# Performance work log

Measured on AMD Instinct MI355X. Metric: run time of the kernel, lower is better.

## Reference

```python
import jax, jax.numpy as jnp
import numpy as np

N = 100_000      # nodes
E = 1_600_000    # edges (avg degree 16)
H = 4            # heads
C = 32           # per-head channels
HID = 128        # hidden = H*C
L = 4            # layers
IN, ED, OUT = 8, 6, 256
NEG_SLOPE = 0.2  # LeakyReLU default in GATv2Conv


def setup_inputs() -> dict:
    key = jax.random.key(0)
    ks = jax.random.split(key, 16)
    s = 0.1
    return {
        "x": jax.random.normal(ks[0], (N, IN), dtype=jnp.float32),
        "edge_index": jax.random.randint(ks[1], (2, E), 0, N, dtype=jnp.int32),
        "edge_attr": jax.random.normal(ks[2], (E, ED), dtype=jnp.float32),
        "W_in": jax.random.normal(ks[3], (IN, HID), dtype=jnp.float32) * s,
        "b_in": jnp.zeros((HID,), jnp.float32),
        "W_l": jax.random.normal(ks[4], (L, HID, HID), dtype=jnp.float32) * s,
        "b_l": jnp.zeros((L, HID), jnp.float32),
        "W_r": jax.random.normal(ks[5], (L, HID, HID), dtype=jnp.float32) * s,
        "b_r": jnp.zeros((L, HID), jnp.float32),
        "W_e": jax.random.normal(ks[6], (L, ED, HID), dtype=jnp.float32) * s,
        "att": jax.random.normal(ks[7], (L, H, C), dtype=jnp.float32) * s,
        "bias": jnp.zeros((L, HID), jnp.float32),
        "ln_w": jnp.ones((L, HID), jnp.float32),
        "ln_b": jnp.zeros((L, HID), jnp.float32),
        "W_out": jax.random.normal(ks[8], (HID, OUT), dtype=jnp.float32) * s,
        "b_out": jnp.zeros((OUT,), jnp.float32),
    }


def _elu(x):
    return jnp.where(x > 0, x, jnp.expm1(x))


def _leaky(x):
    return jnp.where(x > 0, x, NEG_SLOPE * x)


def _layernorm(x, w, b):
    mu = jnp.mean(x, axis=-1, keepdims=True)
    var = jnp.var(x, axis=-1, keepdims=True)
    return (x - mu) * jax.lax.rsqrt(var + 1e-5) * w + b


def _forward(x, edge_index, edge_attr, W_in, b_in, W_l, b_l, W_r, b_r,
             W_e, att, bias, ln_w, ln_b, W_out, b_out):
    src, dst = edge_index[0], edge_index[1]
    # add_self_loops with fill_value='mean': self-loop edge_attr = mean of incoming edge_attr
    deg = jax.ops.segment_sum(jnp.ones((E,), x.dtype), dst, num_segments=N)
    loop_attr = jax.ops.segment_sum(edge_attr, dst, num_segments=N) / jnp.maximum(deg, 1.0)[:, None]
    loops = jnp.arange(N, dtype=src.dtype)
    src_a = jnp.concatenate([src, loops])          # [E+N]
    dst_a = jnp.concatenate([dst, loops])          # [E+N]
    eattr_a = jnp.concatenate([edge_attr, loop_attr], axis=0)  # [E+N, ED]

    h = _elu(x @ W_in + b_in)  # [N, HID]
    for i in range(L):
        res = h
        xl = (h @ W_l[i] + b_l[i]).reshape(N, H, C)   # source transform
        xr = (h @ W_r[i] + b_r[i]).reshape(N, H, C)   # target transform
        ea = (eattr_a @ W_e[i]).reshape(-1, H, C)     # edge transform
        m = _leaky(xl[src_a] + xr[dst_a] + ea)        # [E+N, H, C]
        score = jnp.einsum('ehc,hc->eh', m, att[i])   # [E+N, H]
        # segment softmax over incoming edges per target node
        smax = jax.ops.segment_max(score, dst_a, num_segments=N)[dst_a]
        ex = jnp.exp(score - smax)
        denom = jax.ops.segment_sum(ex, dst_a, num_segments=N)[dst_a]
        alpha = ex / denom                             # [E+N, H]
        out = jax.ops.segment_sum(alpha[:, :, None] * xl[src_a], dst_a,
                                  num_segments=N).reshape(N, HID) + bias[i]
        h = _elu(_layernorm(out + res, ln_w[i], ln_b[i]))
        # dropout: identity (eval mode)
    return h @ W_out + b_out  # [N, OUT]


def reference(x, edge_index, edge_attr, W_in, b_in, W_l, b_l, W_r, b_r,
              W_e, att, bias, ln_w, ln_b, W_out, b_out):
    return _forward(x, edge_index, edge_attr, W_in, b_in, W_l, b_l, W_r, b_r,
                    W_e, att, bias, ln_w, ln_b, W_out, b_out)
```

## Files before the change

kernel.cpp:

```cpp
#include <hip/hip_runtime.h>
#include <hip/hip_bf16.h>
#include <hip/hip_fp16.h>

#define N_NODES 100000
#define N_EDGES 1600000
#define HEADS 4
#define CHN 32
#define HID 128
#define LAYERS 4
#define IN_F 8
#define ED_F 6
#define OUT_F 256
#define NEG_SLOPE 0.2f

#define NT_GEMM ((N_NODES + 63) / 64)
#define GRID_GEMM 512

typedef _Float16 f16x8 __attribute__((ext_vector_type(8)));
typedef _Float16 f16x4 __attribute__((ext_vector_type(4)));
typedef _Float16 h2 __attribute__((ext_vector_type(2)));
typedef float f32x4 __attribute__((ext_vector_type(4)));

#if defined(__has_builtin)
#if __has_builtin(__builtin_amdgcn_fdot2)
#define HAVE_FDOT2 1
#endif
#endif

__device__ __forceinline__ float elu_f(float x) {
    return x > 0.f ? x : expm1f(x);
}

__device__ __forceinline__ h2 bith2(float f) {
    union { float f; h2 h; } u; u.f = f; return u.h;
}

__device__ __forceinline__ float dot6(h2 e01, h2 e23, h2 e45, const h2* w) {
#ifdef HAVE_FDOT2
    return __builtin_amdgcn_fdot2(e45, w[2],
           __builtin_amdgcn_fdot2(e23, w[1],
           __builtin_amdgcn_fdot2(e01, w[0], 0.f, false), false), false);
#else
    float s = (float)e01[0] * (float)w[0][0];
    s = fmaf((float)e01[1], (float)w[0][1], s);
    s = fmaf((float)e23[0], (float)w[1][0], s);
    s = fmaf((float)e23[1], (float)w[1][1], s);
    s = fmaf((float)e45[0], (float)w[2][0], s);
    s = fmaf((float)e45[1], (float)w[2][1], s);
    return s;
#endif
}


__global__ void hist_kernel(const int* __restrict__ dst, int* __restrict__ fill) {
    int e = blockIdx.x * blockDim.x + threadIdx.x;
    if (e < N_EDGES) atomicAdd(&fill[dst[e]], 1);
}

__global__ void scan1_kernel(const int* __restrict__ cnt, int* __restrict__ bsum) {
    __shared__ int sd[256];
    int t = threadIdx.x;
    int base = blockIdx.x * 1024 + t * 4;
    int s = 0;
#pragma unroll
    for (int j = 0; j < 4; ++j) {
        int i = base + j;
        if (i < N_NODES) s += cnt[i];
    }
    sd[t] = s;
    for (int off = 128; off > 0; off >>= 1) {
        __syncthreads();
        if (t < off) sd[t] += sd[t + off];
    }
    if (t == 0) bsum[blockIdx.x] = sd[0];
}

__global__ void scan2_kernel(int* __restrict__ bsum, int* __restrict__ rowptr, int nb) {
    __shared__ int sd[256];
    int t = threadIdx.x;
    int v = (t < nb) ? bsum[t] : 0;
    sd[t] = v;
    __syncthreads();
    for (int off = 1; off < 256; off <<= 1) {
        int x = (t >= off) ? sd[t - off] : 0;
        __syncthreads();
        sd[t] += x;
        __syncthreads();
    }
    if (t < nb) bsum[t] = sd[t] - v;
    if (t == 0) rowptr[N_NODES] = sd[255];
}

__global__ void scan3_kernel(const int* __restrict__ cnt, const int* __restrict__ bsum,
                             int* __restrict__ rowptr) {
    __shared__ int sd[256];
    int t = threadIdx.x;
    int base = blockIdx.x * 1024 + t * 4;
    int v[4];
#pragma unroll
    for (int j = 0; j < 4; ++j) {
        int i = base + j;
        v[j] = (i < N_NODES) ? cnt[i] : 0;
    }
    int s = v[0] + v[1] + v[2] + v[3];
    sd[t] = s;
    __syncthreads();
    for (int off = 1; off < 256; off <<= 1) {
        int xv = (t >= off) ? sd[t - off] : 0;
        __syncthreads();
        sd[t] += xv;
        __syncthreads();
    }
    int excl = sd[t] - s + bsum[blockIdx.x];
    int pre = 0;
#pragma unroll
    for (int j = 0; j < 4; ++j) {
        int i = base + j;
        if (i < N_NODES) rowptr[i] = excl + pre;
        pre += v[j];
    }
}

__global__ void fill_kernel(const int* __restrict__ src, const int* __restrict__ dst,
                            const int* __restrict__ rowptr, int* __restrict__ fill,
                            int2* __restrict__ csr) {
    int e = blockIdx.x * blockDim.x + threadIdx.x;
    if (e >= N_EDGES) return;
    int d = dst[e];
    int p = rowptr[d] + atomicAdd(&fill[d], 1);
    csr[p] = make_int2(src[e] * 512, e * 16);
}

__global__ void ecvt_kernel(const float* __restrict__ eattr, __half* __restrict__ ea16) {
    int gid = blockIdx.x * blockDim.x + threadIdx.x;
    if (gid >= N_EDGES * 8) return;
    int e = gid >> 3, d = gid & 7;
    float v = (d < ED_F) ? eattr[e * ED_F + d] : 0.f;
    ea16[gid] = __float2half_rn(v);
}

__global__ void lattr_kernel(const int* __restrict__ rowptr, const int2* __restrict__ csr,
                             const __half* __restrict__ ea16, __half* __restrict__ lat16) {
    int gid = blockIdx.x * blockDim.x + threadIdx.x;
    if (gid >= N_NODES * 8) return;
    int n = gid >> 3;
    int d = gid & 7;
    float s = 0.f;
    if (d < ED_F) {
        int rp0 = rowptr[n], rp1 = rowptr[n + 1];
        for (int p = rp0; p < rp1; ++p) {
            int eid = csr[p].y >> 4;
            s += (float)ea16[(size_t)eid * 8 + d];
        }
        int deg = rp1 - rp0;
        s /= (float)(deg > 0 ? deg : 1);
    }
    lat16[gid] = __float2half_rn(s);
}


__global__ void convw_kernel(const float* __restrict__ W_l, const float* __restrict__ W_r,
                             const float* __restrict__ W_out, __half* __restrict__ wbt) {
    int gid = blockIdx.x * blockDim.x + threadIdx.x;
    if (gid >= 5 * 256 * 128) return;
    int b = gid >> 15;
    int idx = gid & 32767;
    int n = idx >> 7, k = idx & 127;
    float val;
    if (b < 4)
        val = (n < HID) ? W_l[b * HID * HID + k * HID + n]
                        : W_r[b * HID * HID + k * HID + (n - HID)];
    else
        val = W_out[k * OUT_F + n];
    int boff = n * 256 + ((k * 2) ^ ((n & 7) << 4));
    *(__half*)((char*)wbt + (size_t)b * 65536 + boff) = __float2half_rn(val);
}


__global__ void in_kernel(const float* __restrict__ x, const float* __restrict__ Wi,
                          const float* __restrict__ bi, __half* __restrict__ h16) {
    int gid = blockIdx.x * blockDim.x + threadIdx.x;
    if (gid >= N_NODES * HID) return;
    int n = gid >> 7, j = gid & 127;
    float acc = bi[j];
#pragma unroll
    for (int k = 0; k < IN_F; ++k) acc = fmaf(x[n * IN_F + k], Wi[k * HID + j], acc);
    h16[gid] = __float2half_rn(elu_f(acc));
}


#define LDS_B_OFF 16384

template <int MODE>
__global__ __launch_bounds__(256, 2) void gemm_kernel(
    const __half* __restrict__ A16, const __half* __restrict__ Bt,
    const float* __restrict__ bias0, const float* __restrict__ bias1,
    __half* __restrict__ xlr16, float* __restrict__ outp) {
    __shared__ __align__(16) unsigned char smem[81920];
    int t = threadIdx.x;

#pragma unroll
    for (int it = 0; it < 16; ++it) {
        int off = (it * 256 + t) * 16;
        *(float4*)(smem + LDS_B_OFF + off) = *(const float4*)((const char*)Bt + off);
    }

    int wave = t >> 6;
    int lane = t & 63;
    int lc = lane & 15, lr = lane >> 4;
    int cbase = wave * 64;

    for (int tile = blockIdx.x; tile < NT_GEMM; tile += GRID_GEMM) {
        int row0 = tile * 64;
#pragma unroll
        for (int it = 0; it < 4; ++it) {
            int idx = it * 256 + t;
            int r = idx >> 4;
            int kb = (idx & 15) * 16;
            f16x8 p = *(const f16x8*)((const char*)A16 + (size_t)(row0 + r) * 256 + kb);
            *(f16x8*)(smem + r * 256 + (kb ^ ((r & 7) << 4))) = p;
        }
        __syncthreads();

        f32x4 acc[4][4];
#pragma unroll
        for (int i = 0; i < 4; ++i)
#pragma unroll
            for (int j = 0; j < 4; ++j) acc[i][j] = (f32x4){0.f, 0.f, 0.f, 0.f};

#pragma unroll
        for (int kk = 0; kk < 4; ++kk) {
            int kb = kk * 64 + lr * 16;
            f16x8 av[4], bv[4];
#pragma unroll
            for (int rt = 0; rt < 4; ++rt) {
                int r = rt * 16 + lc;
                av[rt] = *(const f16x8*)(smem + r * 256 + (kb ^ ((r & 7) << 4)));
            }
#pragma unroll
            for (int ct = 0; ct < 4; ++ct) {
                int c = cbase + ct * 16 + lc;
                bv[ct] = *(const f16x8*)(smem + LDS_B_OFF + c * 256 + (kb ^ ((c & 7) << 4)));
            }
#pragma unroll
            for (int rt = 0; rt < 4; ++rt)
#pragma unroll
                for (int ct = 0; ct < 4; ++ct)
                    acc[rt][ct] = __builtin_amdgcn_mfma_f32_16x16x32_f16(av[rt], bv[ct],
                                                                         acc[rt][ct], 0, 0, 0);
        }
        __syncthreads();

#pragma unroll
        for (int ct = 0; ct < 4; ++ct) {
            int col = cbase + ct * 16 + lc;
            float bv;
            if (MODE == 0) bv = (col < HID) ? bias0[col] : bias1[col - HID];
            else bv = bias0[col];
#pragma unroll
            for (int rt = 0; rt < 4; ++rt) {
#pragma unroll
                for (int q = 0; q < 4; ++q) {
                    int node = row0 + rt * 16 + lr * 4 + q;
                    if (node < N_NODES) {
                        float val = acc[rt][ct][q] + bv;
                        if (MODE == 0)
                            xlr16[(size_t)node * 256 + col] = __float2half_rn(val);
                        else
                            outp[(size_t)node * OUT_F + col] = val;
                    }
                }
            }
        }
    }
}


struct Slot {
    float4 er;
    float2 xv;
};

__device__ __forceinline__ void slot_issue(Slot& s, int i, int total, int rp0,
                                           const int2* __restrict__ csr,
                                           const char* eab, const char* lat16v,
                                           const char* xlb, int vbytes) {
    i = min(i, total - 1);
    const char* eb;
    const char* xb;
    if (i == 0) {
        eb = lat16v;
        xb = xlb + (size_t)vbytes;
    } else {
        int2 se = csr[rp0 + i - 1];
        eb = eab + (size_t)se.y;
        xb = xlb + (size_t)se.x;
    }
    s.er = *(const float4*)eb;
    s.xv = *(const float2*)xb;
}

__device__ __forceinline__ void slot_consume(const Slot& sl, int i, int total,
                                             const h2 we_h2[4][3], const float* attv,
                                             const float* xrv,
                                             float& denom, float* acc) {
    h2 e01 = bith2(sl.er.x), e23 = bith2(sl.er.y), e45 = bith2(sl.er.z);
    h2 x01 = bith2(sl.xv.x), x23 = bith2(sl.xv.y);
    float xf[4];
    xf[0] = (float)x01[0]; xf[1] = (float)x01[1];
    xf[2] = (float)x23[0]; xf[3] = (float)x23[1];
    float t = 0.f;
#pragma unroll
    for (int c = 0; c < 4; ++c) {
        float ea = dot6(e01, e23, e45, we_h2[c]);
        float m = xf[c] + xrv[c] + ea;
        m = m > 0.f ? m : NEG_SLOPE * m;
        t = fmaf(m, attv[c], t);
    }
    t += __shfl_xor(t, 1);
    t += __shfl_xor(t, 2);
    t += __shfl_xor(t, 4);
    float ex = __expf(t);
    ex = (i < total) ? ex : 0.f;
    denom += ex;
#pragma unroll
    for (int c = 0; c < 4; ++c) acc[c] = fmaf(ex, xf[c], acc[c]);
}

__global__ __launch_bounds__(64, 8) void edge_kernel(
    const __half* __restrict__ xlr16,
    __half* __restrict__ h16,
    const int* __restrict__ rowptr, const int2* __restrict__ csr,
    const __half* __restrict__ ea16, const __half* __restrict__ lat16,
    const float* __restrict__ We, const float* __restrict__ att,
    const float* __restrict__ bias_l, const float* __restrict__ lnw,
    const float* __restrict__ lnb) {
    int v = blockIdx.x;
    int lane = threadIdx.x;
    int half = lane >> 5;
    int hl = lane & 31;
    int c0 = hl * 4;

    h2 we_h2[4][3];
#pragma unroll
    for (int c = 0; c < 4; ++c)
#pragma unroll
        for (int d = 0; d < 3; ++d) {
            h2 w;
            w[0] = (_Float16)We[(2 * d) * HID + c0 + c];
            w[1] = (_Float16)We[(2 * d + 1) * HID + c0 + c];
            we_h2[c][d] = w;
        }
    float4 at4 = *(const float4*)(att + c0);
    float attv[4] = {at4.x, at4.y, at4.z, at4.w};
    float xrv[4];
    {
        float2 xraw = *(const float2*)(xlr16 + (size_t)v * 256 + 128 + c0);
        h2 xr01 = bith2(xraw.x), xr23 = bith2(xraw.y);
        xrv[0] = (float)xr01[0]; xrv[1] = (float)xr01[1];
        xrv[2] = (float)xr23[0]; xrv[3] = (float)xr23[1];
    }

    int rp0 = rowptr[v], rp1 = rowptr[v + 1];
    int total = (rp1 - rp0) + 1;
    int R = (total + 1) >> 1;

    const char* xlb = (const char*)xlr16 + (size_t)c0 * 2;
    const char* eab = (const char*)ea16;
    const char* lat16v = (const char*)lat16 + (size_t)v * 16;
    int vbytes = v * 512;

    float denom = 0.f;
    float acc[4] = {0.f, 0.f, 0.f, 0.f};

    Slot sA, sB;
    slot_issue(sA, half, total, rp0, csr, eab, lat16v, xlb, vbytes);
    if (R > 1) slot_issue(sB, 2 + half, total, rp0, csr, eab, lat16v, xlb, vbytes);
    int r = 0;
    for (; r + 2 <= R; r += 2) {
        slot_consume(sA, 2 * r + half, total, we_h2, attv, xrv, denom, acc);
        if (r + 2 < R) slot_issue(sA, 2 * (r + 2) + half, total, rp0, csr, eab, lat16v, xlb, vbytes);
        slot_consume(sB, 2 * (r + 1) + half, total, we_h2, attv, xrv, denom, acc);
        if (r + 3 < R) slot_issue(sB, 2 * (r + 3) + half, total, rp0, csr, eab, lat16v, xlb, vbytes);
    }
    if (r < R) slot_consume(sA, 2 * r + half, total, we_h2, attv, xrv, denom, acc);

    denom += __shfl_xor(denom, 32);
#pragma unroll
    for (int c = 0; c < 4; ++c) acc[c] += __shfl_xor(acc[c], 32);

    float rd = 1.f / denom;

    float2 rb = *(const float2*)(h16 + (size_t)v * HID + c0);
    h2 r01 = bith2(rb.x), r23 = bith2(rb.y);
    float4 bv4 = *(const float4*)(bias_l + c0);
    float y[4];
    y[0] = acc[0] * rd + bv4.x + (float)r01[0];
    y[1] = acc[1] * rd + bv4.y + (float)r01[1];
    y[2] = acc[2] * rd + bv4.z + (float)r23[0];
    y[3] = acc[3] * rd + bv4.w + (float)r23[1];
    float s = y[0] + y[1] + y[2] + y[3];
    float sq = fmaf(y[0], y[0], fmaf(y[1], y[1], fmaf(y[2], y[2], y[3] * y[3])));
#pragma unroll
    for (int off = 1; off < 32; off <<= 1) {
        s += __shfl_xor(s, off);
        sq += __shfl_xor(sq, off);
    }
    float mu = s * (1.f / HID);
    float var = sq * (1.f / HID) - mu * mu;
    float rstd = rsqrtf(var + 1e-5f);
    float4 wv4 = *(const float4*)(lnw + c0);
    float4 lb4 = *(const float4*)(lnb + c0);
    if (half == 0) {
        f16x4 o;
        o[0] = (_Float16)elu_f((y[0] - mu) * rstd * wv4.x + lb4.x);
        o[1] = (_Float16)elu_f((y[1] - mu) * rstd * wv4.y + lb4.y);
        o[2] = (_Float16)elu_f((y[2] - mu) * rstd * wv4.z + lb4.z);
        o[3] = (_Float16)elu_f((y[3] - mu) * rstd * wv4.w + lb4.w);
        *(f16x4*)(h16 + (size_t)v * HID + c0) = o;
    }
}


extern "C" void kernel_launch(void* const* d_in, const int* in_sizes, int n_in,
                              void* d_out, int out_size, void* d_ws, size_t ws_size,
                              hipStream_t stream) {
    const float* x     = (const float*)d_in[0];
    const int*   ei    = (const int*)d_in[1];
    const float* eattr = (const float*)d_in[2];
    const float* W_in  = (const float*)d_in[3];
    const float* b_in  = (const float*)d_in[4];
    const float* W_l   = (const float*)d_in[5];
    const float* b_l   = (const float*)d_in[6];
    const float* W_r   = (const float*)d_in[7];
    const float* b_r   = (const float*)d_in[8];
    const float* W_e   = (const float*)d_in[9];
    const float* att   = (const float*)d_in[10];
    const float* bias  = (const float*)d_in[11];
    const float* lnw   = (const float*)d_in[12];
    const float* lnb   = (const float*)d_in[13];
    const float* W_out = (const float*)d_in[14];
    const float* b_out = (const float*)d_in[15];
    float* out = (float*)d_out;

    __half* h16   = (__half*)d_ws;
    __half* lat16 = h16 + (size_t)N_NODES * HID;
    int* rowptr   = (int*)(lat16 + (size_t)N_NODES * 8);
    int* fill     = rowptr + (N_NODES + 4);
    int2* csr     = (int2*)(fill + N_NODES);
    int* bsum     = (int*)(csr + N_EDGES);
    __half* wbt   = (__half*)(bsum + 256);

    __half* xlr16 = (__half*)out;
    __half* ea16  = xlr16 + (size_t)N_NODES * 256;

    const int* srcv = ei;
    const int* dstv = ei + N_EDGES;

    hipMemsetAsync(fill, 0, N_NODES * sizeof(int), stream);
    hist_kernel<<<(N_EDGES + 255) / 256, 256, 0, stream>>>(dstv, fill);
    int nb = (N_NODES + 1023) / 1024;
    scan1_kernel<<<nb, 256, 0, stream>>>(fill, bsum);
    scan2_kernel<<<1, 256, 0, stream>>>(bsum, rowptr, nb);
    scan3_kernel<<<nb, 256, 0, stream>>>(fill, bsum, rowptr);
    hipMemsetAsync(fill, 0, N_NODES * sizeof(int), stream);
    fill_kernel<<<(N_EDGES + 255) / 256, 256, 0, stream>>>(srcv, dstv, rowptr, fill, csr);
    ecvt_kernel<<<(N_EDGES * 8 + 255) / 256, 256, 0, stream>>>(eattr, ea16);
    lattr_kernel<<<(N_NODES * 8 + 255) / 256, 256, 0, stream>>>(rowptr, csr, ea16, lat16);

    convw_kernel<<<(5 * 256 * 128 + 255) / 256, 256, 0, stream>>>(W_l, W_r, W_out, wbt);
    in_kernel<<<(N_NODES * HID) / 256, 256, 0, stream>>>(x, W_in, b_in, h16);

    for (int l = 0; l < LAYERS; ++l) {
        gemm_kernel<0><<<GRID_GEMM, 256, 0, stream>>>(
            h16, wbt + (size_t)l * 32768, b_l + (size_t)l * HID, b_r + (size_t)l * HID,
            xlr16, nullptr);
        edge_kernel<<<N_NODES, 64, 0, stream>>>(
            xlr16, h16, rowptr, csr, ea16, lat16,
            W_e + (size_t)l * ED_F * HID, att + (size_t)l * HEADS * CHN,
            bias + (size_t)l * HID, lnw + (size_t)l * HID, lnb + (size_t)l * HID);
    }

    gemm_kernel<1><<<GRID_GEMM, 256, 0, stream>>>(
        h16, wbt + (size_t)4 * 32768, b_out, nullptr, nullptr, out);
}
```

Measured before the change: 925.4 us.

## Compute GATv2 edge message math in packed fp16 with duplicated edge attributes

Edge attributes are now stored with each feature value duplicated as a half2 pair (32 bytes per edge), so the edge kernel can form the message with packed fp16 multiply-adds over channel pairs. The older form did one fdot2 per channel. LeakyReLU becomes a packed max, the attention dot uses fdot2, and the softmax uses exp2 with log2(e) folded into the attention weights. This cuts per-edge ALU work in the edge kernel. In exchange, the edge-attribute buffer doubles in size and each edge costs extra gather bandwidth, and the pre-activation sum is accumulated in fp16, which loses precision.

```diff
diff --git a/kernel.cpp b/kernel.cpp
--- a/kernel.cpp
+++ b/kernel.cpp
@@ -35,19 +35,11 @@
     union { float f; h2 h; } u; u.f = f; return u.h;
 }
 
-__device__ __forceinline__ float dot6(h2 e01, h2 e23, h2 e45, const h2* w) {
+__device__ __forceinline__ float fdot2f(h2 a, h2 b, float c) {
 #ifdef HAVE_FDOT2
-    return __builtin_amdgcn_fdot2(e45, w[2],
-           __builtin_amdgcn_fdot2(e23, w[1],
-           __builtin_amdgcn_fdot2(e01, w[0], 0.f, false), false), false);
+    return __builtin_amdgcn_fdot2(a, b, c, false);
 #else
-    float s = (float)e01[0] * (float)w[0][0];
-    s = fmaf((float)e01[1], (float)w[0][1], s);
-    s = fmaf((float)e23[0], (float)w[1][0], s);
-    s = fmaf((float)e23[1], (float)w[1][1], s);
-    s = fmaf((float)e45[0], (float)w[2][0], s);
-    s = fmaf((float)e45[1], (float)w[2][1], s);
-    return s;
+    return fmaf((float)a[1], (float)b[1], fmaf((float)a[0], (float)b[0], c));
 #endif
 }
 
@@ -128,13 +120,13 @@
     if (e >= N_EDGES) return;
     int d = dst[e];
     int p = rowptr[d] + atomicAdd(&fill[d], 1);
-    csr[p] = make_int2(src[e] * 512, e * 16);
+    csr[p] = make_int2(src[e] * 512, e * 32);
 }
 
 __global__ void ecvt_kernel(const float* __restrict__ eattr, __half* __restrict__ ea16) {
     int gid = blockIdx.x * blockDim.x + threadIdx.x;
-    if (gid >= N_EDGES * 8) return;
-    int e = gid >> 3, d = gid & 7;
+    if (gid >= N_EDGES * 16) return;
+    int e = gid >> 4, d = (gid & 15) >> 1;
     float v = (d < ED_F) ? eattr[e * ED_F + d] : 0.f;
     ea16[gid] = __float2half_rn(v);
 }
@@ -142,15 +134,16 @@
 __global__ void lattr_kernel(const int* __restrict__ rowptr, const int2* __restrict__ csr,
                              const __half* __restrict__ ea16, __half* __restrict__ lat16) {
     int gid = blockIdx.x * blockDim.x + threadIdx.x;
-    if (gid >= N_NODES * 8) return;
-    int n = gid >> 3;
-    int d = gid & 7;
+    if (gid >= N_NODES * 16) return;
+    int n = gid >> 4;
+    int j = gid & 15;
+    int d = j >> 1;
     float s = 0.f;
     if (d < ED_F) {
         int rp0 = rowptr[n], rp1 = rowptr[n + 1];
         for (int p = rp0; p < rp1; ++p) {
-            int eid = csr[p].y >> 4;
-            s += (float)ea16[(size_t)eid * 8 + d];
+            int eid = csr[p].y >> 5;
+            s += (float)ea16[(size_t)eid * 16 + 2 * d];
         }
         int deg = rp1 - rp0;
         s /= (float)(deg > 0 ? deg : 1);
@@ -277,7 +270,8 @@
 
 
 struct Slot {
-    float4 er;
+    float4 er0;
+    float2 er1;
     float2 xv;
 };
 
@@ -296,35 +290,38 @@
         eb = eab + (size_t)se.y;
         xb = xlb + (size_t)se.x;
     }
-    s.er = *(const float4*)eb;
+    s.er0 = *(const float4*)eb;
+    s.er1 = *(const float2*)(eb + 16);
     s.xv = *(const float2*)xb;
 }
 
 __device__ __forceinline__ void slot_consume(const Slot& sl, int i, int total,
-                                             const h2 we_h2[4][3], const float* attv,
-                                             const float* xrv,
-                                             float& denom, float* acc) {
-    h2 e01 = bith2(sl.er.x), e23 = bith2(sl.er.y), e45 = bith2(sl.er.z);
-    h2 x01 = bith2(sl.xv.x), x23 = bith2(sl.xv.y);
-    float xf[4];
-    xf[0] = (float)x01[0]; xf[1] = (float)x01[1];
-    xf[2] = (float)x23[0]; xf[3] = (float)x23[1];
-    float t = 0.f;
-#pragma unroll
-    for (int c = 0; c < 4; ++c) {
-        float ea = dot6(e01, e23, e45, we_h2[c]);
-        float m = xf[c] + xrv[c] + ea;
-        m = m > 0.f ? m : NEG_SLOPE * m;
-        t = fmaf(m, attv[c], t);
-    }
+                                             const h2 w2[6][2], const h2* att2,
+                                             const h2* xr2, float& denom, float* acc) {
+    h2 xl0 = bith2(sl.xv.x), xl1 = bith2(sl.xv.y);
+    h2 sp0 = xl0 + xr2[0];
+    h2 sp1 = xl1 + xr2[1];
+    h2 es;
+    es = bith2(sl.er0.x); sp0 += es * w2[0][0]; sp1 += es * w2[0][1];
+    es = bith2(sl.er0.y); sp0 += es * w2[1][0]; sp1 += es * w2[1][1];
+    es = bith2(sl.er0.z); sp0 += es * w2[2][0]; sp1 += es * w2[2][1];
+    es = bith2(sl.er0.w); sp0 += es * w2[3][0]; sp1 += es * w2[3][1];
+    es = bith2(sl.er1.x); sp0 += es * w2[4][0]; sp1 += es * w2[4][1];
+    es = bith2(sl.er1.y); sp0 += es * w2[5][0]; sp1 += es * w2[5][1];
+    const h2 kns = {(_Float16)NEG_SLOPE, (_Float16)NEG_SLOPE};
+    h2 l0 = __builtin_elementwise_max(sp0, sp0 * kns);
+    h2 l1 = __builtin_elementwise_max(sp1, sp1 * kns);
+    float t = fdot2f(l1, att2[1], fdot2f(l0, att2[0], 0.f));
     t += __shfl_xor(t, 1);
     t += __shfl_xor(t, 2);
     t += __shfl_xor(t, 4);
-    float ex = __expf(t);
+    float ex = exp2f(t);
     ex = (i < total) ? ex : 0.f;
     denom += ex;
-#pragma unroll
-    for (int c = 0; c < 4; ++c) acc[c] = fmaf(ex, xf[c], acc[c]);
+    acc[0] = fmaf((float)xl0[0], ex, acc[0]);
+    acc[1] = fmaf((float)xl0[1], ex, acc[1]);
+    acc[2] = fmaf((float)xl1[0], ex, acc[2]);
+    acc[3] = fmaf((float)xl1[1], ex, acc[3]);
 }
 
 __global__ __launch_bounds__(64, 8) void edge_kernel(
@@ -341,24 +338,29 @@
     int hl = lane & 31;
     int c0 = hl * 4;
 
-    h2 we_h2[4][3];
-#pragma unroll
-    for (int c = 0; c < 4; ++c)
-#pragma unroll
-        for (int d = 0; d < 3; ++d) {
+    h2 w2[6][2];
+#pragma unroll
+    for (int d = 0; d < 6; ++d)
+#pragma unroll
+        for (int p = 0; p < 2; ++p) {
             h2 w;
-            w[0] = (_Float16)We[(2 * d) * HID + c0 + c];
-            w[1] = (_Float16)We[(2 * d + 1) * HID + c0 + c];
-            we_h2[c][d] = w;
+            w[0] = (_Float16)We[d * HID + c0 + 2 * p];
+            w[1] = (_Float16)We[d * HID + c0 + 2 * p + 1];
+            w2[d][p] = w;
         }
-    float4 at4 = *(const float4*)(att + c0);
-    float attv[4] = {at4.x, at4.y, at4.z, at4.w};
-    float xrv[4];
+    const float L2E = 1.44269504f;
+    h2 att2[2];
+    {
+        float4 a = *(const float4*)(att + c0);
+        h2 t0, t1;
+        t0[0] = (_Float16)(a.x * L2E); t0[1] = (_Float16)(a.y * L2E);
+        t1[0] = (_Float16)(a.z * L2E); t1[1] = (_Float16)(a.w * L2E);
+        att2[0] = t0; att2[1] = t1;
+    }
+    h2 xr2[2];
     {
         float2 xraw = *(const float2*)(xlr16 + (size_t)v * 256 + 128 + c0);
-        h2 xr01 = bith2(xraw.x), xr23 = bith2(xraw.y);
-        xrv[0] = (float)xr01[0]; xrv[1] = (float)xr01[1];
-        xrv[2] = (float)xr23[0]; xrv[3] = (float)xr23[1];
+        xr2[0] = bith2(xraw.x); xr2[1] = bith2(xraw.y);
     }
 
     int rp0 = rowptr[v], rp1 = rowptr[v + 1];
@@ -367,7 +369,7 @@
 
     const char* xlb = (const char*)xlr16 + (size_t)c0 * 2;
     const char* eab = (const char*)ea16;
-    const char* lat16v = (const char*)lat16 + (size_t)v * 16;
+    const char* lat16v = (const char*)lat16 + (size_t)v * 32;
     int vbytes = v * 512;
 
     float denom = 0.f;
@@ -378,12 +380,12 @@
     if (R > 1) slot_issue(sB, 2 + half, total, rp0, csr, eab, lat16v, xlb, vbytes);
     int r = 0;
     for (; r + 2 <= R; r += 2) {
-        slot_consume(sA, 2 * r + half, total, we_h2, attv, xrv, denom, acc);
+        slot_consume(sA, 2 * r + half, total, w2, att2, xr2, denom, acc);
         if (r + 2 < R) slot_issue(sA, 2 * (r + 2) + half, total, rp0, csr, eab, lat16v, xlb, vbytes);
-        slot_consume(sB, 2 * (r + 1) + half, total, we_h2, attv, xrv, denom, acc);
+        slot_consume(sB, 2 * (r + 1) + half, total, w2, att2, xr2, denom, acc);
         if (r + 3 < R) slot_issue(sB, 2 * (r + 3) + half, total, rp0, csr, eab, lat16v, xlb, vbytes);
     }
-    if (r < R) slot_consume(sA, 2 * r + half, total, we_h2, attv, xrv, denom, acc);
+    if (r < R) slot_consume(sA, 2 * r + half, total, w2, att2, xr2, denom, acc);
 
     denom += __shfl_xor(denom, 32);
 #pragma unroll
@@ -445,7 +447,7 @@
 
     __half* h16   = (__half*)d_ws;
     __half* lat16 = h16 + (size_t)N_NODES * HID;
-    int* rowptr   = (int*)(lat16 + (size_t)N_NODES * 8);
+    int* rowptr   = (int*)(lat16 + (size_t)N_NODES * 16);
     int* fill     = rowptr + (N_NODES + 4);
     int2* csr     = (int2*)(fill + N_NODES);
     int* bsum     = (int*)(csr + N_EDGES);
@@ -465,8 +467,8 @@
     scan3_kernel<<<nb, 256, 0, stream>>>(fill, bsum, rowptr);
     hipMemsetAsync(fill, 0, N_NODES * sizeof(int), stream);
     fill_kernel<<<(N_EDGES + 255) / 256, 256, 0, stream>>>(srcv, dstv, rowptr, fill, csr);
-    ecvt_kernel<<<(N_EDGES * 8 + 255) / 256, 256, 0, stream>>>(eattr, ea16);
-    lattr_kernel<<<(N_NODES * 8 + 255) / 256, 256, 0, stream>>>(rowptr, csr, ea16, lat16);
+    ecvt_kernel<<<(N_EDGES * 16 + 255) / 256, 256, 0, stream>>>(eattr, ea16);
+    lattr_kernel<<<(N_NODES * 16 + 255) / 256, 256, 0, stream>>>(rowptr, csr, ea16, lat16);
 
     convw_kernel<<<(5 * 256 * 128 + 255) / 256, 256, 0, stream>>>(W_l, W_r, W_out, wbt);
     in_kernel<<<(N_NODES * HID) / 256, 256, 0, stream>>>(x, W_in, b_in, h16);
```

Result: slower. 997.3 us (+7.8%).
